# Kernel optimization log

Hardware: AMD Instinct MI355X
Metric: run time of the kernel (lower is better)

## Reference

```python
import jax, jax.numpy as jnp
import numpy as np

N = 50000      # nodes
E = 800000     # edges
F_IN = 512     # num_features
H = 128        # hidden


def setup_inputs() -> dict:
    key = jax.random.key(0)
    ks = jax.random.split(key, 10)
    edge_index = jax.random.randint(ks[0], (2, E), 0, N, dtype=jnp.int64 if jax.config.jax_enable_x64 else jnp.int32)
    x = jax.random.normal(ks[1], (N, F_IN), jnp.float32)
    weights = jax.random.uniform(ks[2], (E,), jnp.float32)
    def w(i, shape, fan):
        return jax.random.normal(ks[i], shape, jnp.float32) / np.sqrt(fan).astype(np.float32)
    return {
        "edge_index": edge_index,
        "x": x,
        "weights": weights,
        "W_lin1": w(3, (F_IN, H), F_IN), "b_lin1": jnp.zeros((H,), jnp.float32),
        "W_conv1": w(4, (H, 2 * H), H), "b_conv1": jnp.zeros((2 * H,), jnp.float32),
        "W_mu": w(5, (2 * H, H), 2 * H), "b_mu": jnp.zeros((H,), jnp.float32),
        "W_lin": w(6, (2 * H, 1), 2 * H), "b_lin": jnp.zeros((1,), jnp.float32),
    }


def gcn_conv(x, W, b, src, dst, ew, n):
    """PyG GCNConv with edge weights: add self-loops (weight 1), symmetric norm, scatter-add."""
    loop = jnp.arange(n, dtype=src.dtype)
    s2 = jnp.concatenate([src, loop])
    d2 = jnp.concatenate([dst, loop])
    w2 = jnp.concatenate([ew, jnp.ones((n,), x.dtype)])
    deg = jax.ops.segment_sum(w2, d2, num_segments=n)          # weighted in-degree incl. self-loop
    dinv = jnp.where(deg > 0, deg, 1.0) ** -0.5
    dinv = jnp.where(deg > 0, dinv, 0.0)
    norm = dinv[s2] * w2 * dinv[d2]                            # [E+N]
    h = x @ W                                                   # [N, out]
    out = jax.ops.segment_sum(h[s2] * norm[:, None], d2, num_segments=n)
    return out + b


def reference(edge_index, x, weights, W_lin1, b_lin1, W_conv1, b_conv1, W_mu, b_mu, W_lin, b_lin):
    n = x.shape[0]
    src, dst = edge_index[0], edge_index[1]
    # eval mode: dropout is identity, VGAE.encode returns mu
    h = x @ W_lin1 + b_lin1                                     # lin1
    h = jax.nn.relu(gcn_conv(h, W_conv1, b_conv1, src, dst, weights, n))
    z = gcn_conv(h, W_mu, b_mu, src, dst, weights, n)           # mu == embeddings
    emb_edges = jnp.concatenate([z[src], z[dst]], axis=1)       # [E, 2H]
    out = jax.nn.sigmoid(emb_edges @ W_lin + b_lin)
    return out.squeeze(-1)                                      # [E]
```

## Files before the change

### kernel.cpp

```cpp
#include <hip/hip_runtime.h>
#include <hip/hip_bf16.h>
#include <math.h>


#define NSL 256
#define RSH 8
#define RNG 256

typedef __attribute__((ext_vector_type(8))) short bf16x8;
typedef __attribute__((ext_vector_type(4))) float f32x4;

typedef const __attribute__((address_space(1))) unsigned int* gas_t;
typedef __attribute__((address_space(3))) unsigned int* las_t;

static __device__ __forceinline__ void gload_lds16(const void* g, void* l) {
    __builtin_amdgcn_global_load_lds((gas_t)g, (las_t)l, 16, 0, 0);
}

static __device__ __forceinline__ ushort f2b(float f) {
    __hip_bfloat16 h = __float2bfloat16(f);
    return *(ushort*)&h;
}
static __device__ __forceinline__ float b2f(ushort u) {
    unsigned int v = ((unsigned int)u) << 16;
    return *(float*)&v;
}
static __device__ __forceinline__ bf16x8 cvt8(float4 a, float4 b) {
    bf16x8 r;
    r[0] = (short)f2b(a.x); r[1] = (short)f2b(a.y); r[2] = (short)f2b(a.z); r[3] = (short)f2b(a.w);
    r[4] = (short)f2b(b.x); r[5] = (short)f2b(b.y); r[6] = (short)f2b(b.z); r[7] = (short)f2b(b.w);
    return r;
}


__global__ __launch_bounds__(256) void bucket_count(const int* __restrict__ dst,
                                                    int* __restrict__ cntA, int E, int NR) {
    __shared__ int lc[256];
    const int b = blockIdx.x, t = threadIdx.x;
    lc[t] = 0;
    __syncthreads();
    const int beg = (int)((long long)b * E / NSL);
    const int end = (int)((long long)(b + 1) * E / NSL);
    for (int e = beg + t; e < end; e += 256) atomicAdd(&lc[dst[e] >> RSH], 1);
    __syncthreads();
    if (t < NR) cntA[b * NR + t] = lc[t];
}

__global__ __launch_bounds__(256) void range_scan(int* __restrict__ cntA,
                                                  int* __restrict__ rtot, int NR) {
    __shared__ int s_[256];
    const int r = blockIdx.x, t = threadIdx.x;
    int v = cntA[t * NR + r];
    s_[t] = v;
    __syncthreads();
    for (int off = 1; off < 256; off <<= 1) {
        int add = (t >= off) ? s_[t - off] : 0;
        __syncthreads();
        s_[t] += add;
        __syncthreads();
    }
    cntA[t * NR + r] = s_[t] - v;
    if (t == 255) rtot[r] = s_[t];
}

__global__ __launch_bounds__(256) void base_scan(const int* __restrict__ rtot,
                                                 int* __restrict__ baseOut, int NR) {
    __shared__ int s_[256];
    const int t = threadIdx.x;
    int v = (t < NR) ? rtot[t] : 0;
    s_[t] = v;
    __syncthreads();
    for (int off = 1; off < 256; off <<= 1) {
        int add = (t >= off) ? s_[t - off] : 0;
        __syncthreads();
        s_[t] += add;
        __syncthreads();
    }
    if (t < NR) baseOut[t] = s_[t] - v;
    if (t == NR - 1) baseOut[NR] = s_[t];
}

__global__ __launch_bounds__(256) void bucket_scatter(const int* __restrict__ src,
                                                      const int* __restrict__ dst,
                                                      const float* __restrict__ w,
                                                      const int* __restrict__ cntA,
                                                      const int* __restrict__ baseOut,
                                                      uint2* __restrict__ rec, int E, int NR) {
    __shared__ int cur[256];
    const int b = blockIdx.x, t = threadIdx.x;
    if (t < NR) cur[t] = cntA[b * NR + t] + baseOut[t];
    __syncthreads();
    const int beg = (int)((long long)b * E / NSL);
    const int end = (int)((long long)(b + 1) * E / NSL);
    for (int e = beg + t; e < end; e += 256) {
        int d = dst[e];
        int r = d >> RSH;
        int pos = atomicAdd(&cur[r], 1);
        rec[pos] = make_uint2(((unsigned int)(d & (RNG - 1)) << 24) | (unsigned int)src[e],
                              __float_as_uint(w[e]));
    }
}

__global__ __launch_bounds__(256) void range_build(const uint2* __restrict__ rec,
                                                   const int* __restrict__ baseOut,
                                                   float* __restrict__ dinv,
                                                   int* __restrict__ offs,
                                                   uint2* __restrict__ ce,
                                                   int N, int E) {
    __shared__ float lw[256];
    __shared__ int lc[256];
    __shared__ int sc[256];
    const int r = blockIdx.x, t = threadIdx.x;
    lw[t] = 0.f; lc[t] = 0;
    __syncthreads();
    const int beg = baseOut[r], end = baseOut[r + 1];
    for (int e = beg + t; e < end; e += 256) {
        uint2 pk = rec[e];
        int dl = pk.x >> 24;
        atomicAdd(&lc[dl], 1);
        atomicAdd(&lw[dl], __uint_as_float(pk.y));
    }
    __syncthreads();
    int v = lc[t];
    sc[t] = v;
    __syncthreads();
    for (int off = 1; off < 256; off <<= 1) {
        int add = (t >= off) ? sc[t - off] : 0;
        __syncthreads();
        sc[t] += add;
        __syncthreads();
    }
    const int node = (r << RSH) + t;
    const int o = beg + sc[t] - v;
    if (node < N) {
        dinv[node] = 1.0f / sqrtf(1.0f + lw[t]);
        offs[node] = o;
    }
    if (r == 0 && t == 0) offs[N] = E;
    lc[t] = o;
    __syncthreads();
    for (int e = beg + t; e < end; e += 256) {
        uint2 pk = rec[e];
        int dl = pk.x >> 24;
        int pos = atomicAdd(&lc[dl], 1);
        ce[pos] = make_uint2(pk.x & 0xFFFFFF, pk.y);
    }
}

__global__ __launch_bounds__(256) void prep_kernel(const float* __restrict__ W1,
                                                   const float* __restrict__ Wc,
                                                   const float* __restrict__ Wm,
                                                   const float* __restrict__ Wl,
                                                   const float* __restrict__ bm,
                                                   ushort* __restrict__ W1T,
                                                   ushort* __restrict__ WcT,
                                                   float* __restrict__ wmp,
                                                   float* __restrict__ wmq,
                                                   float* __restrict__ bpq,
                                                   int F, int H, int H2,
                                                   int nb1, int nb2) {
    const int b = blockIdx.x, t = threadIdx.x;
    if (b < nb1) {
        int i = b * 256 + t;
        if (i < F * H) {
            int k = i / H, n = i % H;
            W1T[(size_t)n * F + k] = f2b(W1[i]);
        }
    } else if (b < nb1 + nb2) {
        int i = (b - nb1) * 256 + t;
        if (i < H * H2) {
            int k = i / H2, n = i % H2;
            WcT[(size_t)n * H + k] = f2b(Wc[i]);
        }
    } else {
        int j = t;
        float sp = 0.f, sq = 0.f;
        for (int k = 0; k < 128; ++k) {
            float v = Wm[(size_t)j * 128 + k];
            sp += v * Wl[k];
            sq += v * Wl[128 + k];
        }
        wmp[j] = sp; wmq[j] = sq;
        if (j == 0) { float s = 0.f; for (int k = 0; k < 128; ++k) s += bm[k] * Wl[k];       bpq[0] = s; }
        if (j == 1) { float s = 0.f; for (int k = 0; k < 128; ++k) s += bm[k] * Wl[128 + k]; bpq[1] = s; }
    }
}

__global__ __launch_bounds__(256) void gemm1_mfma(const float* __restrict__ A,
                                                  const ushort* __restrict__ BT,
                                                  const float* __restrict__ bias,
                                                  const float* __restrict__ dinv,
                                                  ushort* __restrict__ C, int M) {
    __shared__ float  As[64 * 64];
    __shared__ ushort Bs[128 * 64];
    char* AsB = (char*)As;
    char* BsB = (char*)Bs;
    const int t = threadIdx.x;
    const int bm = blockIdx.x * 64;
    const int lane = t & 63;
    const int wid = t >> 6;
    const int wm = (wid >> 1) * 32, wn = (wid & 1) * 64;

    f32x4 acc[2][4] = {};

    const int a_row_l = (lane >> 4);
    const int a_ib    = (lane & 15) * 16;
    const int b_row_l = (lane >> 3);
    const int b_ib    = (lane & 7) * 16;

#pragma unroll 1
    for (int tt = 0; tt < 8; ++tt) {
        const int k0 = tt * 64;
#pragma unroll
        for (int j = 0; j < 4; ++j) {
            int c = wid * 4 + j;
            int row = c * 4 + a_row_l;
            int sw = a_ib ^ ((row & 7) << 5);
            int grow = min(bm + row, M - 1);
            const char* src = (const char*)A + ((size_t)grow * 512 + k0) * 4 + sw;
            gload_lds16(src, AsB + c * 1024);
        }
#pragma unroll
        for (int j = 0; j < 4; ++j) {
            int c = wid * 4 + j;
            int row = c * 8 + b_row_l;
            int sw = b_ib ^ ((row & 7) << 4);
            const char* src = (const char*)BT + (size_t)row * 1024 + k0 * 2 + sw;
            gload_lds16(src, BsB + c * 1024);
        }
        __syncthreads();
#pragma unroll
        for (int ks = 0; ks < 2; ++ks) {
            bf16x8 af[2], bfr[4];
#pragma unroll
            for (int mi = 0; mi < 2; ++mi) {
                int r = wm + mi * 16 + (lane & 15);
                int byte = r * 256 + ks * 128 + (lane >> 4) * 32;
                byte ^= (r & 7) << 5;
                float4 f0 = *(const float4*)(AsB + byte);
                float4 f1 = *(const float4*)(AsB + byte + 16);
                af[mi] = cvt8(f0, f1);
            }
#pragma unroll
            for (int ni = 0; ni < 4; ++ni) {
                int r = wn + ni * 16 + (lane & 15);
                int byte = r * 128 + ks * 64 + (lane >> 4) * 16;
                byte ^= (r & 7) << 4;
                bfr[ni] = *(const bf16x8*)(BsB + byte);
            }
#pragma unroll
            for (int mi = 0; mi < 2; ++mi)
#pragma unroll
                for (int ni = 0; ni < 4; ++ni)
                    acc[mi][ni] = __builtin_amdgcn_mfma_f32_16x16x32_bf16(af[mi], bfr[ni], acc[mi][ni], 0, 0, 0);
        }
        __syncthreads();
    }

#pragma unroll
    for (int mi = 0; mi < 2; ++mi)
#pragma unroll
        for (int r = 0; r < 4; ++r) {
            int row = bm + wm + mi * 16 + (lane >> 4) * 4 + r;
            if (row < M) {
                float dv = dinv[row];
#pragma unroll
                for (int ni = 0; ni < 4; ++ni) {
                    int col = wn + ni * 16 + (lane & 15);
                    C[(size_t)row * 128 + col] = f2b((acc[mi][ni][r] + bias[col]) * dv);
                }
            }
        }
}

__global__ __launch_bounds__(256) void aggregate_bf16(const ushort* __restrict__ hs,
                                                      const int* __restrict__ offs,
                                                      const uint2* __restrict__ ce,
                                                      const float* __restrict__ dinv,
                                                      ushort* __restrict__ out, int n) {
    int node = (int)((blockIdx.x * (size_t)blockDim.x + threadIdx.x) >> 6);
    int lane = threadIdx.x & 63;
    if (node >= n) return;
    unsigned int hv = *(const unsigned int*)(hs + (size_t)node * 128 + lane * 2);
    float ax = b2f((ushort)(hv & 0xffff));
    float ay = b2f((ushort)(hv >> 16));
    int beg = offs[node], end = offs[node + 1];
    for (int e = beg; e < end; e += 8) {
        uint2 rr[8];
#pragma unroll
        for (int j = 0; j < 8; ++j) {
            bool v = (e + j) < end;
            rr[j] = v ? ce[e + j] : make_uint2((unsigned)node, 0u);
        }
        unsigned int vv[8];
#pragma unroll
        for (int j = 0; j < 8; ++j)
            vv[j] = *(const unsigned int*)(hs + (size_t)rr[j].x * 128 + lane * 2);
#pragma unroll
        for (int j = 0; j < 8; ++j) {
            float wj = __uint_as_float(rr[j].y);
            ax += wj * b2f((ushort)(vv[j] & 0xffff));
            ay += wj * b2f((ushort)(vv[j] >> 16));
        }
    }
    float dv = dinv[node];
    unsigned int o = (unsigned int)f2b(ax * dv) | ((unsigned int)f2b(ay * dv) << 16);
    *(unsigned int*)(out + (size_t)node * 128 + lane * 2) = o;
}

__global__ __launch_bounds__(64) void gemm2_stream(const ushort* __restrict__ A,
                                                   const ushort* __restrict__ BT,
                                                   const float* __restrict__ bc,
                                                   const float* __restrict__ wmp,
                                                   const float* __restrict__ wmq,
                                                   const float* __restrict__ dinv,
                                                   float* __restrict__ pe,
                                                   float* __restrict__ qe, int M) {
    const int lane = threadIdx.x;
    const int r0 = blockIdx.x * 16;
    const int lrow = lane & 15;
    const int lk   = (lane >> 4) * 8;

    f32x4 acc[16] = {};

    const ushort* a  = A  + (size_t)min(r0 + lrow, M - 1) * 128 + lk;
    const ushort* bp = BT + (size_t)lrow * 128 + lk;

#pragma unroll
    for (int ks = 0; ks < 4; ++ks) {
        const int k0 = ks * 32;
        bf16x8 af = *(const bf16x8*)(a + k0);
#pragma unroll
        for (int ni = 0; ni < 16; ++ni) {
            bf16x8 bfr = *(const bf16x8*)(bp + (size_t)ni * 16 * 128 + k0);
            acc[ni] = __builtin_amdgcn_mfma_f32_16x16x32_bf16(af, bfr, acc[ni], 0, 0, 0);
        }
    }

    float bcv[16], wpv[16], wqv[16];
#pragma unroll
    for (int ni = 0; ni < 16; ++ni) {
        int col = ni * 16 + lrow;
        bcv[ni] = bc[col];
        wpv[ni] = wmp[col];
        wqv[ni] = wmq[col];
    }
#pragma unroll
    for (int r = 0; r < 4; ++r) {
        float sp = 0.f, sq = 0.f;
#pragma unroll
        for (int ni = 0; ni < 16; ++ni) {
            float h = fmaxf(acc[ni][r] + bcv[ni], 0.f);
            sp += h * wpv[ni];
            sq += h * wqv[ni];
        }
#pragma unroll
        for (int off = 1; off < 16; off <<= 1) {
            sp += __shfl_xor(sp, off);
            sq += __shfl_xor(sq, off);
        }
        if (lrow == 0) {
            int row = r0 + (lane >> 4) * 4 + r;
            if (row < M) {
                float dv = dinv[row];
                pe[row] = sp * dv;
                qe[row] = sq * dv;
            }
        }
    }
}

__global__ __launch_bounds__(256) void agg_scalar(const float* __restrict__ pe,
                                                  const float* __restrict__ qe,
                                                  const int* __restrict__ offs,
                                                  const uint2* __restrict__ ce,
                                                  const float* __restrict__ dinv,
                                                  const float* __restrict__ bpq,
                                                  float* __restrict__ p,
                                                  float* __restrict__ q, int n) {
    int i = blockIdx.x * 256 + threadIdx.x;
    if (i >= n) return;
    float ap = pe[i], aq = qe[i];
    int beg = offs[i], end = offs[i + 1];
    for (int k = beg; k < end; k += 4) {
        uint2 rr[4];
#pragma unroll
        for (int j = 0; j < 4; ++j) {
            bool v = (k + j) < end;
            rr[j] = v ? ce[k + j] : make_uint2((unsigned)i, 0u);
        }
        float pv[4], qv[4];
#pragma unroll
        for (int j = 0; j < 4; ++j) { pv[j] = pe[rr[j].x]; qv[j] = qe[rr[j].x]; }
#pragma unroll
        for (int j = 0; j < 4; ++j) {
            float wj = __uint_as_float(rr[j].y);
            ap += wj * pv[j];
            aq += wj * qv[j];
        }
    }
    float dv = dinv[i];
    p[i] = ap * dv + bpq[0];
    q[i] = aq * dv + bpq[1];
}

__global__ __launch_bounds__(256) void edge_out_kernel(const int* __restrict__ src,
                                                       const int* __restrict__ dst,
                                                       const float* __restrict__ p,
                                                       const float* __restrict__ q,
                                                       const float* __restrict__ bl,
                                                       float* __restrict__ out, int e) {
    int i = blockIdx.x * 256 + threadIdx.x;
    if (i < e) {
        float t = p[src[i]] + q[dst[i]] + bl[0];
        out[i] = 1.0f / (1.0f + expf(-t));
    }
}


extern "C" void kernel_launch(void* const* d_in, const int* in_sizes, int n_in,
                              void* d_out, int out_size, void* d_ws, size_t ws_size,
                              hipStream_t stream) {
    const int*   edge_index = (const int*)d_in[0];
    const float* x   = (const float*)d_in[1];
    const float* w   = (const float*)d_in[2];
    const float* W1  = (const float*)d_in[3];
    const float* b1  = (const float*)d_in[4];
    const float* Wc  = (const float*)d_in[5];
    const float* bc  = (const float*)d_in[6];
    const float* Wm  = (const float*)d_in[7];
    const float* bm  = (const float*)d_in[8];
    const float* Wl  = (const float*)d_in[9];
    const float* bl  = (const float*)d_in[10];
    float* out = (float*)d_out;

    const int E  = in_sizes[2];
    const int H  = in_sizes[4];
    const int F  = in_sizes[3] / H;
    const int N  = in_sizes[1] / F;
    const int H2 = 2 * H;
    const int NR = (N + RNG - 1) / RNG;

    const int* src = edge_index;
    const int* dst = edge_index + E;

    char* ws = (char*)d_ws;
    size_t off = 0;
    auto alloc = [&](size_t bytes) -> void* {
        off = (off + 255) & ~(size_t)255;
        void* r = ws + off;
        off += bytes;
        return r;
    };
    int*    cntA    = (int*)   alloc((size_t)NSL * NR * 4);
    int*    rtot    = (int*)   alloc((size_t)NR * 4);
    int*    baseOut = (int*)   alloc((size_t)(NR + 1) * 4);
    uint2*  rec     = (uint2*) alloc((size_t)E * 8);
    uint2*  ce      = (uint2*) alloc((size_t)E * 8);
    float*  dinv    = (float*) alloc((size_t)N * 4);
    int*    offs    = (int*)   alloc((size_t)(N + 1) * 4);
    ushort* hs_bf   = (ushort*)alloc((size_t)N * H * 2);
    ushort* agg1_bf = (ushort*)alloc((size_t)N * H * 2);
    ushort* W1T     = (ushort*)alloc((size_t)H * F * 2);
    ushort* WcT     = (ushort*)alloc((size_t)H2 * H * 2);
    float*  wmp     = (float*) alloc(H2 * 4);
    float*  wmq     = (float*) alloc(H2 * 4);
    float*  bpq     = (float*) alloc(2 * 4);
    float*  pe      = (float*) alloc((size_t)N * 4);
    float*  qe      = (float*) alloc((size_t)N * 4);
    float*  p       = (float*) alloc((size_t)N * 4);
    float*  q       = (float*) alloc((size_t)N * 4);
    (void)ws_size; (void)n_in; (void)out_size;

    int nbN  = (N + 255) / 256;
    int nbE  = (E + 255) / 256;
    int nbW  = (int)(((size_t)N * 64 + 255) / 256);
    int nb64 = (N + 63) / 64;
    int nb16 = (N + 15) / 16;
    int nb1  = (F * H + 255) / 256;
    int nb2  = (H * H2 + 255) / 256;

    bucket_count<<<NSL, 256, 0, stream>>>(dst, cntA, E, NR);
    range_scan<<<NR, 256, 0, stream>>>(cntA, rtot, NR);
    base_scan<<<1, 256, 0, stream>>>(rtot, baseOut, NR);
    bucket_scatter<<<NSL, 256, 0, stream>>>(src, dst, w, cntA, baseOut, rec, E, NR);
    range_build<<<NR, 256, 0, stream>>>(rec, baseOut, dinv, offs, ce, N, E);

    prep_kernel<<<nb1 + nb2 + 1, 256, 0, stream>>>(W1, Wc, Wm, Wl, bm, W1T, WcT,
                                                   wmp, wmq, bpq, F, H, H2, nb1, nb2);

    gemm1_mfma<<<nb64, 256, 0, stream>>>(x, W1T, b1, dinv, hs_bf, N);
    aggregate_bf16<<<nbW, 256, 0, stream>>>(hs_bf, offs, ce, dinv, agg1_bf, N);
    gemm2_stream<<<nb16, 64, 0, stream>>>(agg1_bf, WcT, bc, wmp, wmq, dinv, pe, qe, N);
    agg_scalar<<<nbN, 256, 0, stream>>>(pe, qe, offs, ce, dinv, bpq, p, q, N);
    edge_out_kernel<<<nbE, 256, 0, stream>>>(src, dst, p, q, bl, out, E);
}
```

Measured before the change: 190.0 us.

## Retile gemm1 to 128 rows with register prefetch and LDS-staged stores

The first GEMM (x @ W_lin1) now takes 128-row tiles instead of 64. Global loads for the next k-slice go into registers while the current slice is computed, replacing the direct global-to-LDS loads. A is converted to bf16 once when written to LDS, not on every fragment read, which halves A's LDS footprint and read traffic. The epilogue stages the output tile in LDS so global stores are coalesced 16-byte writes, at the cost of more registers per thread, fewer blocks, and an extra barrier.

Result: no change. 190.2 us (+0.1%).

```diff
diff --git a/kernel.cpp b/kernel.cpp
--- a/kernel.cpp
+++ b/kernel.cpp
@@ -10,13 +10,6 @@
 typedef __attribute__((ext_vector_type(8))) short bf16x8;
 typedef __attribute__((ext_vector_type(4))) float f32x4;
 
-typedef const __attribute__((address_space(1))) unsigned int* gas_t;
-typedef __attribute__((address_space(3))) unsigned int* las_t;
-
-static __device__ __forceinline__ void gload_lds16(const void* g, void* l) {
-    __builtin_amdgcn_global_load_lds((gas_t)g, (las_t)l, 16, 0, 0);
-}
-
 static __device__ __forceinline__ ushort f2b(float f) {
     __hip_bfloat16 h = __float2bfloat16(f);
     return *(ushort*)&h;
@@ -24,12 +17,6 @@
 static __device__ __forceinline__ float b2f(ushort u) {
     unsigned int v = ((unsigned int)u) << 16;
     return *(float*)&v;
-}
-static __device__ __forceinline__ bf16x8 cvt8(float4 a, float4 b) {
-    bf16x8 r;
-    r[0] = (short)f2b(a.x); r[1] = (short)f2b(a.y); r[2] = (short)f2b(a.z); r[3] = (short)f2b(a.w);
-    r[4] = (short)f2b(b.x); r[5] = (short)f2b(b.y); r[6] = (short)f2b(b.z); r[7] = (short)f2b(b.w);
-    return r;
 }
 
 
@@ -191,65 +178,78 @@
                                                   const float* __restrict__ bias,
                                                   const float* __restrict__ dinv,
                                                   ushort* __restrict__ C, int M) {
-    __shared__ float  As[64 * 64];
-    __shared__ ushort Bs[128 * 64];
-    char* AsB = (char*)As;
-    char* BsB = (char*)Bs;
+    __shared__ ushort S[2 * 128 * 64];
+    ushort* As = S;
+    ushort* Bs = S + 128 * 64;
+    char* SB = (char*)S;
     const int t = threadIdx.x;
-    const int bm = blockIdx.x * 64;
+    const int bm = blockIdx.x * 128;
     const int lane = t & 63;
     const int wid = t >> 6;
-    const int wm = (wid >> 1) * 32, wn = (wid & 1) * 64;
-
-    f32x4 acc[2][4] = {};
-
-    const int a_row_l = (lane >> 4);
-    const int a_ib    = (lane & 15) * 16;
-    const int b_row_l = (lane >> 3);
-    const int b_ib    = (lane & 7) * 16;
+    const int wm = (wid >> 1) * 64, wn = (wid & 1) * 64;
+
+    f32x4 acc[4][4] = {};
+
+    const int arow0 = wid * 32 + (lane >> 4);
+    const int acol  = (lane & 15) * 4;
+    const int brow0 = wid * 32 + (lane >> 3);
+    const int bcol  = (lane & 7) * 8;
+
+    float4 aReg[8];
+    uint4  bReg[4];
+
+    auto issue = [&](int k0) {
+#pragma unroll
+        for (int j = 0; j < 8; ++j) {
+            int row = arow0 + j * 4;
+            bool valid = (bm + row) < M;
+            aReg[j] = valid ? *(const float4*)(A + (size_t)(bm + row) * 512 + k0 + acol)
+                            : make_float4(0.f, 0.f, 0.f, 0.f);
+        }
+#pragma unroll
+        for (int j = 0; j < 4; ++j) {
+            int row = brow0 + j * 8;
+            bReg[j] = *(const uint4*)(BT + (size_t)row * 512 + k0 + bcol);
+        }
+    };
+
+    issue(0);
 
 #pragma unroll 1
     for (int tt = 0; tt < 8; ++tt) {
-        const int k0 = tt * 64;
+#pragma unroll
+        for (int j = 0; j < 8; ++j) {
+            int row = arow0 + j * 4;
+            ushort4 u;
+            u.x = f2b(aReg[j].x); u.y = f2b(aReg[j].y); u.z = f2b(aReg[j].z); u.w = f2b(aReg[j].w);
+            int byte = (row * 128 + acol * 2) ^ ((row & 7) << 4);
+            *(ushort4*)((char*)As + byte) = u;
+        }
 #pragma unroll
         for (int j = 0; j < 4; ++j) {
-            int c = wid * 4 + j;
-            int row = c * 4 + a_row_l;
-            int sw = a_ib ^ ((row & 7) << 5);
-            int grow = min(bm + row, M - 1);
-            const char* src = (const char*)A + ((size_t)grow * 512 + k0) * 4 + sw;
-            gload_lds16(src, AsB + c * 1024);
-        }
-#pragma unroll
-        for (int j = 0; j < 4; ++j) {
-            int c = wid * 4 + j;
-            int row = c * 8 + b_row_l;
-            int sw = b_ib ^ ((row & 7) << 4);
-            const char* src = (const char*)BT + (size_t)row * 1024 + k0 * 2 + sw;
-            gload_lds16(src, BsB + c * 1024);
-        }
+            int row = brow0 + j * 8;
+            int byte = (row * 128 + bcol * 2) ^ ((row & 7) << 4);
+            *(uint4*)((char*)Bs + byte) = bReg[j];
+        }
+        if (tt < 7) issue((tt + 1) * 64);
         __syncthreads();
 #pragma unroll
         for (int ks = 0; ks < 2; ++ks) {
-            bf16x8 af[2], bfr[4];
-#pragma unroll
-            for (int mi = 0; mi < 2; ++mi) {
-                int r = wm + mi * 16 + (lane & 15);
-                int byte = r * 256 + ks * 128 + (lane >> 4) * 32;
-                byte ^= (r & 7) << 5;
-                float4 f0 = *(const float4*)(AsB + byte);
-                float4 f1 = *(const float4*)(AsB + byte + 16);
-                af[mi] = cvt8(f0, f1);
+            bf16x8 af[4], bfr[4];
+#pragma unroll
+            for (int mi = 0; mi < 4; ++mi) {
+                int row = wm + mi * 16 + (lane & 15);
+                int byte = (row * 128 + ks * 64 + (lane >> 4) * 16) ^ ((row & 7) << 4);
+                af[mi] = *(bf16x8*)((char*)As + byte);
             }
 #pragma unroll
             for (int ni = 0; ni < 4; ++ni) {
-                int r = wn + ni * 16 + (lane & 15);
-                int byte = r * 128 + ks * 64 + (lane >> 4) * 16;
-                byte ^= (r & 7) << 4;
-                bfr[ni] = *(const bf16x8*)(BsB + byte);
+                int row = wn + ni * 16 + (lane & 15);
+                int byte = (row * 128 + ks * 64 + (lane >> 4) * 16) ^ ((row & 7) << 4);
+                bfr[ni] = *(bf16x8*)((char*)Bs + byte);
             }
 #pragma unroll
-            for (int mi = 0; mi < 2; ++mi)
+            for (int mi = 0; mi < 4; ++mi)
 #pragma unroll
                 for (int ni = 0; ni < 4; ++ni)
                     acc[mi][ni] = __builtin_amdgcn_mfma_f32_16x16x32_bf16(af[mi], bfr[ni], acc[mi][ni], 0, 0, 0);
@@ -257,20 +257,34 @@
         __syncthreads();
     }
 
-#pragma unroll
-    for (int mi = 0; mi < 2; ++mi)
+    float bcv[4];
+#pragma unroll
+    for (int ni = 0; ni < 4; ++ni) bcv[ni] = bias[wn + ni * 16 + (lane & 15)];
+#pragma unroll
+    for (int mi = 0; mi < 4; ++mi)
 #pragma unroll
         for (int r = 0; r < 4; ++r) {
-            int row = bm + wm + mi * 16 + (lane >> 4) * 4 + r;
-            if (row < M) {
-                float dv = dinv[row];
-#pragma unroll
-                for (int ni = 0; ni < 4; ++ni) {
-                    int col = wn + ni * 16 + (lane & 15);
-                    C[(size_t)row * 128 + col] = f2b((acc[mi][ni][r] + bias[col]) * dv);
-                }
+            int row = wm + mi * 16 + (lane >> 4) * 4 + r;
+            int grow = bm + row;
+            float dv = (grow < M) ? dinv[grow] : 0.f;
+#pragma unroll
+            for (int ni = 0; ni < 4; ++ni) {
+                int col = wn + ni * 16 + (lane & 15);
+                int byte = (row * 256 + col * 2) ^ ((row & 7) << 4);
+                *(ushort*)(SB + byte) = f2b((acc[mi][ni][r] + bcv[ni]) * dv);
             }
         }
+    __syncthreads();
+#pragma unroll
+    for (int it = 0; it < 8; ++it) {
+        int idx = it * 256 + t;
+        int row = idx >> 4;
+        int grow = bm + row;
+        if (grow < M) {
+            int byte = (row * 256 + (idx & 15) * 16) ^ ((row & 7) << 4);
+            *(uint4*)(C + (size_t)grow * 128 + (idx & 15) * 8) = *(const uint4*)(SB + byte);
+        }
+    }
 }
 
 __global__ __launch_bounds__(256) void aggregate_bf16(const ushort* __restrict__ hs,
@@ -472,13 +486,13 @@
     float*  q       = (float*) alloc((size_t)N * 4);
     (void)ws_size; (void)n_in; (void)out_size;
 
-    int nbN  = (N + 255) / 256;
-    int nbE  = (E + 255) / 256;
-    int nbW  = (int)(((size_t)N * 64 + 255) / 256);
-    int nb64 = (N + 63) / 64;
-    int nb16 = (N + 15) / 16;
-    int nb1  = (F * H + 255) / 256;
-    int nb2  = (H * H2 + 255) / 256;
+    int nbN   = (N + 255) / 256;
+    int nbE   = (E + 255) / 256;
+    int nbW   = (int)(((size_t)N * 64 + 255) / 256);
+    int nb128 = (N + 127) / 128;
+    int nb16  = (N + 15) / 16;
+    int nb1   = (F * H + 255) / 256;
+    int nb2   = (H * H2 + 255) / 256;
 
     bucket_count<<<NSL, 256, 0, stream>>>(dst, cntA, E, NR);
     range_scan<<<NR, 256, 0, stream>>>(cntA, rtot, NR);
@@ -489,7 +503,7 @@
     prep_kernel<<<nb1 + nb2 + 1, 256, 0, stream>>>(W1, Wc, Wm, Wl, bm, W1T, WcT,
                                                    wmp, wmq, bpq, F, H, H2, nb1, nb2);
 
-    gemm1_mfma<<<nb64, 256, 0, stream>>>(x, W1T, b1, dinv, hs_bf, N);
+    gemm1_mfma<<<nb128, 256, 0, stream>>>(x, W1T, b1, dinv, hs_bf, N);
     aggregate_bf16<<<nbW, 256, 0, stream>>>(hs_bf, offs, ce, dinv, agg1_bf, N);
     gemm2_stream<<<nb16, 64, 0, stream>>>(agg1_bf, WcT, bc, wmp, wmq, dinv, pe, qe, N);
     agg_scalar<<<nbN, 256, 0, stream>>>(pe, qe, offs, ce, dinv, bpq, p, q, N);
```
